# Kernel optimization log

Hardware: AMD Instinct MI355X
Metric: run time of the kernel (lower is better)

The kernel has to match this reference:

```python
import jax, jax.numpy as jnp
import numpy as np

HIDDEN = 128
K = 20
T = 20000
N_PTS = 10011


def setup_inputs() -> dict:
    key = jax.random.key(0)
    ks = jax.random.split(key, 20)
    points = jax.random.normal(ks[0], (N_PTS, 3), dtype=jnp.float32)
    triangles = jax.random.randint(ks[1], (T, 3), 0, N_PTS, dtype=jnp.int64)
    init_probs = jax.random.uniform(ks[2], (T,), dtype=jnp.float32)
    s = 0.05
    inp = {"points": points, "triangles": triangles, "init_probs": init_probs}
    for li in range(3):
        inp[f"W1_{li}"] = jax.random.normal(ks[3 + 4 * li], (HIDDEN, HIDDEN + 9), dtype=jnp.float32) * s
        inp[f"b1_{li}"] = jnp.zeros((HIDDEN,), dtype=jnp.float32)
        inp[f"W2_{li}"] = jax.random.normal(ks[4 + 4 * li], (HIDDEN, HIDDEN), dtype=jnp.float32) * s
        inp[f"b2_{li}"] = jnp.zeros((HIDDEN,), dtype=jnp.float32)
    inp["Wf"] = jax.random.normal(ks[15], (1, HIDDEN), dtype=jnp.float32) * s
    inp["bf"] = jnp.zeros((1,), dtype=jnp.float32)
    return inp


def _geometry(points, triangles):
    tp = points[triangles]                      # [T, 3verts, 3xyz]
    e_ij = tp[:, 0] - tp[:, 1]
    e_ik = tp[:, 0] - tp[:, 2]
    e_jk = tp[:, 1] - tp[:, 2]
    ev = jnp.stack([e_ij, e_ik, e_jk], axis=1)  # [T, 3, 3]
    t_max = jnp.max(ev, axis=1)                 # [T, 3]
    t_min = jnp.min(ev, axis=1)                 # [T, 3]
    bary = tp.mean(axis=1)                      # [T, 3]
    return t_min, t_max, bary


def _knn_edges(bary, k):
    # squared distances (monotone in cdist) -> same k smallest neighbors
    sq = jnp.sum(bary * bary, axis=1)
    d2 = sq[:, None] + sq[None, :] - 2.0 * (bary @ bary.T)   # [T, T]
    _, idx = jax.lax.top_k(-d2, k + 1)                       # k+1 smallest
    nbr = idx[:, 1:]                                         # drop self
    t = bary.shape[0]
    src = jnp.repeat(jnp.arange(t, dtype=nbr.dtype), k)      # [T*k]
    tgt = nbr.reshape(-1)                                    # [T*k]
    return src, tgt


def _triconv(x, t_min, t_max, bary, src, tgt, W1, b1, W2, b2):
    r_n_k = jnp.concatenate(
        [t_min[src] - t_min[tgt], t_max[src] - t_max[tgt], bary[src] - bary[tgt]],
        axis=1,
    )                                                        # [E, 9]
    h = jnp.concatenate([r_n_k, x[src] - x[tgt]], axis=1)    # [E, H+9]
    h = jax.nn.relu(h @ W1.T + b1) @ W2.T + b2               # [E, H]
    return jax.ops.segment_sum(h, src, num_segments=x.shape[0])


def reference(points, triangles, init_probs,
              W1_0, b1_0, W2_0, b2_0,
              W1_1, b1_1, W2_1, b2_1,
              W1_2, b1_2, W2_2, b2_2,
              Wf, bf):
    t_min, t_max, bary = _geometry(points, triangles)
    k = min(K, triangles.shape[0] - 1)
    src, tgt = _knn_edges(bary, k)
    feats = jnp.broadcast_to(init_probs[:, None], (init_probs.shape[0], HIDDEN))
    feats = _triconv(feats, t_min, t_max, bary, src, tgt, W1_0, b1_0, W2_0, b2_0)
    feats = _triconv(feats, t_min, t_max, bary, src, tgt, W1_1, b1_1, W2_1, b2_1)
    feats = _triconv(feats, t_min, t_max, bary, src, tgt, W1_2, b1_2, W2_2, b2_2)
    logits = (feats @ Wf.T + bf)[:, 0]
    return jax.nn.sigmoid(logits)
```

## Files before the change

### kernel.cpp

```cpp
#include <hip/hip_runtime.h>
#include <math.h>

#define T_TRI 20000
#define KNN_K 20
#define H     128

#define WS_GEO    0
#define WS_BQ     (1u<<20)
#define WS_NBR    (2u<<20)
#define WS_RS     (4u<<20)
#define WS_MT     ((4u<<20)+4096)
#define WS_WV     ((4u<<20)+4096+(256u<<10))
#define WS_MM     (5u<<20)
#define WS_CSTART ((5u<<20)+64)
#define WS_CPTR   ((5u<<20)+(32u<<10))
#define WS_HIST   ((5u<<20)+(64u<<10))
#define WS_CID    ((5u<<20)+(128u<<10))
#define WS_CSORT  ((5u<<20)+(256u<<10))
#define WS_OID    ((5u<<20)+(384u<<10))
#define WS_BQS    ((5u<<20)+(512u<<10))
#define WS_WA     ((5u<<20)+(840u<<10))
#define WS_PS     (6u<<20)
#define WS_GEOS   (7u<<20)
#define WS_ZB     (9u<<20)
#define WS_ZA     (20u<<20)

__device__ __forceinline__ float readlane_f(float v, int l) {
    return __uint_as_float(__builtin_amdgcn_readlane(__float_as_uint(v), l));
}
__device__ __forceinline__ unsigned encf(float f) {
    unsigned u = __float_as_uint(f);
    return (u & 0x80000000u) ? ~u : (u | 0x80000000u);
}
__device__ __forceinline__ float decf(unsigned e) {
    unsigned u = (e & 0x80000000u) ? (e & 0x7FFFFFFFu) : ~e;
    return __uint_as_float(u);
}
__device__ __forceinline__ int xcd_swz(int bid, int nwg) {
    int q = nwg >> 3, rm = nwg & 7;
    int x = bid & 7, idx = bid >> 3;
    return (x < rm) ? x*(q+1) + idx : rm*(q+1) + (x-rm)*q + idx;
}

__global__ void grid_init_kernel(unsigned* __restrict__ hist, unsigned* __restrict__ mm) {
    int i = blockIdx.x * 256 + threadIdx.x;
    if (i < 4096) hist[i] = 0u;
    if (i < 3) mm[i] = 0xFFFFFFFFu;
    if (i >= 3 && i < 6) mm[i] = 0u;
}

__global__ void geom_kernel(const float* __restrict__ pts, const int* __restrict__ tris,
                            float* __restrict__ geo, float4* __restrict__ bq,
                            unsigned* __restrict__ mm) {
    int t = blockIdx.x * blockDim.x + threadIdx.x;
    int lane = threadIdx.x & 63;
    bool act = (t < T_TRI);
    int tt = act ? t : 0;
    int i0 = tris[3*tt], i1 = tris[3*tt+1], i2 = tris[3*tt+2];
    float ax = pts[3*i0], ay = pts[3*i0+1], az = pts[3*i0+2];
    float bx = pts[3*i1], by = pts[3*i1+1], bz = pts[3*i1+2];
    float cx = pts[3*i2], cy = pts[3*i2+1], cz = pts[3*i2+2];
    float e0x = ax-bx, e0y = ay-by, e0z = az-bz;
    float e1x = ax-cx, e1y = ay-cy, e1z = az-cz;
    float e2x = bx-cx, e2y = by-cy, e2z = bz-cz;
    float mnx = fminf(fminf(e0x,e1x),e2x), mny = fminf(fminf(e0y,e1y),e2y), mnz = fminf(fminf(e0z,e1z),e2z);
    float mxx = fmaxf(fmaxf(e0x,e1x),e2x), mxy = fmaxf(fmaxf(e0y,e1y),e2y), mxz = fmaxf(fmaxf(e0z,e1z),e2z);
    float gx = (ax+bx+cx)*(1.0f/3.0f), gy = (ay+by+cy)*(1.0f/3.0f), gz = (az+bz+cz)*(1.0f/3.0f);
    float sq = (gx*gx + gy*gy) + gz*gz;
    if (act) {
        float* g = geo + (size_t)t*12;
        g[0]=mnx; g[1]=mny; g[2]=mnz; g[3]=mxx; g[4]=mxy; g[5]=mxz;
        g[6]=gx;  g[7]=gy;  g[8]=gz;  g[9]=0.f; g[10]=0.f; g[11]=0.f;
        bq[t] = make_float4(gx, gy, gz, sq);
    }
    unsigned n0 = act ? encf(gx) : 0xFFFFFFFFu;
    unsigned n1 = act ? encf(gy) : 0xFFFFFFFFu;
    unsigned n2 = act ? encf(gz) : 0xFFFFFFFFu;
    unsigned x0 = act ? encf(gx) : 0u;
    unsigned x1 = act ? encf(gy) : 0u;
    unsigned x2 = act ? encf(gz) : 0u;
#pragma unroll
    for (int off = 32; off >= 1; off >>= 1) {
        n0 = min(n0, (unsigned)__shfl_xor((int)n0, off));
        n1 = min(n1, (unsigned)__shfl_xor((int)n1, off));
        n2 = min(n2, (unsigned)__shfl_xor((int)n2, off));
        x0 = max(x0, (unsigned)__shfl_xor((int)x0, off));
        x1 = max(x1, (unsigned)__shfl_xor((int)x1, off));
        x2 = max(x2, (unsigned)__shfl_xor((int)x2, off));
    }
    if (lane == 0) {
        atomicMin(&mm[0], n0); atomicMin(&mm[1], n1); atomicMin(&mm[2], n2);
        atomicMax(&mm[3], x0); atomicMax(&mm[4], x1); atomicMax(&mm[5], x2);
    }
}

__global__ void cellhist_kernel(const float4* __restrict__ bq, const unsigned* __restrict__ mm,
                                int* __restrict__ cellid, unsigned* __restrict__ hist) {
    int t = blockIdx.x * 256 + threadIdx.x;
    if (t >= T_TRI) return;
    float mnx = decf(mm[0]), mny = decf(mm[1]), mnz = decf(mm[2]);
    float mxx = decf(mm[3]), mxy = decf(mm[4]), mxz = decf(mm[5]);
    float ihx = 16.f / fmaxf(mxx-mnx, 1e-30f);
    float ihy = 16.f / fmaxf(mxy-mny, 1e-30f);
    float ihz = 16.f / fmaxf(mxz-mnz, 1e-30f);
    float4 b = bq[t];
    int ix = min(15, max(0, (int)((b.x-mnx)*ihx)));
    int iy = min(15, max(0, (int)((b.y-mny)*ihy)));
    int iz = min(15, max(0, (int)((b.z-mnz)*ihz)));
    int c = (ix<<8) | (iy<<4) | iz;
    cellid[t] = c;
    atomicAdd(&hist[c], 1u);
}

__global__ __launch_bounds__(1024) void prefix_kernel(const unsigned* __restrict__ hist,
                                                      unsigned* __restrict__ cellstart,
                                                      unsigned* __restrict__ cellptr) {
    __shared__ unsigned sbuf[1024];
    int tid = threadIdx.x;
    uint4 v = ((const uint4*)hist)[tid];
    unsigned mysum = v.x + v.y + v.z + v.w;
    sbuf[tid] = mysum;
    __syncthreads();
    for (int off = 1; off < 1024; off <<= 1) {
        unsigned add = (tid >= off) ? sbuf[tid - off] : 0u;
        __syncthreads();
        sbuf[tid] += add;
        __syncthreads();
    }
    unsigned excl = sbuf[tid] - mysum;
    unsigned p0 = excl, p1 = p0 + v.x, p2 = p1 + v.y, p3 = p2 + v.z;
    cellstart[4*tid+0] = p0; cellstart[4*tid+1] = p1;
    cellstart[4*tid+2] = p2; cellstart[4*tid+3] = p3;
    cellptr[4*tid+0] = p0; cellptr[4*tid+1] = p1;
    cellptr[4*tid+2] = p2; cellptr[4*tid+3] = p3;
    if (tid == 1023) cellstart[4096] = p3 + v.w;
}

__global__ void scatter_kernel(const float4* __restrict__ bq, const int* __restrict__ cellid,
                               const float* __restrict__ geo, const float* __restrict__ probs,
                               unsigned* __restrict__ cellptr, float4* __restrict__ bqs,
                               int* __restrict__ oid, int* __restrict__ csort,
                               float* __restrict__ geo_s, float* __restrict__ probs_s) {
    int t = blockIdx.x * 256 + threadIdx.x;
    if (t >= T_TRI) return;
    int c = cellid[t];
    unsigned p = atomicAdd(&cellptr[c], 1u);
    bqs[p] = bq[t];
    oid[p]  = t;
    csort[p] = c;
    const float4* g4 = (const float4*)geo;
    float4* g4s = (float4*)geo_s;
    g4s[(size_t)p*3+0] = g4[(size_t)t*3+0];
    g4s[(size_t)p*3+1] = g4[(size_t)t*3+1];
    g4s[(size_t)p*3+2] = g4[(size_t)t*3+2];
    probs_s[p] = probs[t];
}

__global__ __launch_bounds__(256) void knn_grid_kernel(const float4* __restrict__ bqs,
        const int* __restrict__ oid, const int* __restrict__ csort,
        const unsigned* __restrict__ cellstart, const unsigned* __restrict__ mm,
        int* __restrict__ nbr) {
    int wave = threadIdx.x >> 6, lane = threadIdx.x & 63;
    int r = blockIdx.x * 4 + wave;
    float4 q = bqs[r];
    int myc = csort[r];
    int cx = (myc>>8)&15, cy = (myc>>4)&15, cz = myc&15;
    float mnx = decf(mm[0]), mny = decf(mm[1]), mnz = decf(mm[2]);
    float hx = (decf(mm[3]) - mnx) * (1.f/16.f);
    float hy = (decf(mm[4]) - mny) * (1.f/16.f);
    float hz = (decf(mm[5]) - mnz) * (1.f/16.f);
    float hmin = fminf(hx, fminf(hy, hz));

    float rd = INFINITY;
    int   ri = 0x7FF00000 | lane;
    int   rk = lane;
    float th = INFINITY;
    int   mi = 0x7FFFFFFF;

#define SCAN_RANGE(RS, RE)                                                          \
    for (unsigned base = (RS); base < (RE); base += 64u) {                          \
        unsigned k = base + (unsigned)lane;                                         \
        bool kv = (k < (RE));                                                       \
        float4 c4 = kv ? bqs[k] : make_float4(INFINITY,INFINITY,INFINITY,INFINITY); \
        int ov = kv ? oid[k] : 0x7FFFFFFF;                                          \
        float dot = fmaf(q.z, c4.z, fmaf(q.y, c4.y, q.x*c4.x));                     \
        float d = (q.w + c4.w) - 2.0f*dot;                                          \
        unsigned long long bal = __ballot(kv && (d <= th));                         \
        while (bal) {                                                               \
            int src = __ffsll(bal) - 1; bal &= bal - 1;                             \
            float dc = readlane_f(d, src);                                          \
            int   jc = __builtin_amdgcn_readlane(ov, src);                          \
            int   kc = (int)base + src;                                             \
            if ((dc < th) || (dc == th && jc < mi)) {                               \
                bool less = (rd < dc) || (rd == dc && ri < jc);                     \
                int pos = __popcll(__ballot(less) & 0x1FFFFFull);                   \
                float sd = __shfl_up(rd, 1);                                        \
                int   si = __shfl_up(ri, 1);                                        \
                int   sk = __shfl_up(rk, 1);                                        \
                if (lane < 21) {                                                    \
                    if (lane == pos)      { rd = dc; ri = jc; rk = kc; }            \
                    else if (lane > pos)  { rd = sd; ri = si; rk = sk; }            \
                }                                                                   \
                th = readlane_f(rd, 20);                                            \
                mi = __builtin_amdgcn_readlane(ri, 20);                             \
            }                                                                       \
        }                                                                           \
    }

#define CELL_BOUND_OK(EX, EY, EZ)                                                   \
    ({  float cl0 = fmaf((float)(EX), hx, mnx);                                     \
        float cm0 = fmaf((float)(EY), hy, mny);                                     \
        float cn0 = fmaf((float)(EZ), hz, mnz);                                     \
        float ddx = fmaxf(fmaxf(cl0 - q.x, q.x - (cl0 + hx)), 0.f);                 \
        float ddy = fmaxf(fmaxf(cm0 - q.y, q.y - (cm0 + hy)), 0.f);                 \
        float ddz = fmaxf(fmaxf(cn0 - q.z, q.z - (cn0 + hz)), 0.f);                 \
        float bnd = fmaf(ddx, ddx, fmaf(ddy, ddy, ddz*ddz));                        \
        (bnd <= th + 1e-3f); })

    {
        unsigned hs = cellstart[myc], he = cellstart[myc + 1];
        unsigned k64 = hs + (unsigned)lane;
        bool kv = (k64 < he);
        float4 c4 = kv ? bqs[k64] : make_float4(INFINITY,INFINITY,INFINITY,INFINITY);
        float dot = fmaf(q.z, c4.z, fmaf(q.y, c4.y, q.x*c4.x));
        float d = (q.w + c4.w) - 2.0f*dot;
        int   jx = kv ? oid[k64] : (0x7FF00000 | lane);
        int   kc = kv ? (int)k64 : 0;
        if (!kv) d = INFINITY;
#pragma unroll
        for (int kk = 2; kk <= 64; kk <<= 1) {
#pragma unroll
            for (int jj = kk >> 1; jj >= 1; jj >>= 1) {
                float od = __shfl_xor(d, jj);
                int   oj = __shfl_xor(jx, jj);
                int   ok = __shfl_xor(kc, jj);
                bool up    = ((lane & kk) == 0);
                bool lower = ((lane & jj) == 0);
                bool less  = (d < od) || (d == od && jx < oj);
                bool keep  = ((lower == up) ? less : !less);
                d = keep ? d : od; jx = keep ? jx : oj; kc = keep ? kc : ok;
            }
        }
        rd = d; ri = jx; rk = kc;
        th = readlane_f(rd, 20);
        mi = __builtin_amdgcn_readlane(ri, 20);
        if (hs + 64u < he) { SCAN_RANGE(hs + 64u, he) }
    }

    for (int w = 1; w <= 15; ++w) {
        if (w == 1) {
            int i = lane;
            bool val = (i < 27) && (i != 13);
            int ii = (i < 27) ? i : 0;
            int dz = ii % 3 - 1, dy = (ii / 3) % 3 - 1, dx = ii / 9 - 1;
            int ex = cx + dx, ey = cy + dy, ez = cz + dz;
            val = val && ex >= 0 && ex < 16 && ey >= 0 && ey < 16 && ez >= 0 && ez < 16;
            int cell = (ex<<8) | (ey<<4) | ez;
            unsigned cs = 0u, ce = 0u;
            if (val) { cs = cellstart[cell]; ce = cellstart[cell+1]; }
            val = val && (cs < ce);
            if (val) val = CELL_BOUND_OK(ex, ey, ez);
            unsigned long long cm = __ballot(val);
            while (cm) {
                int cl = __ffsll(cm) - 1; cm &= cm - 1;
                unsigned s0 = (unsigned)__builtin_amdgcn_readlane((int)cs, cl);
                unsigned e0 = (unsigned)__builtin_amdgcn_readlane((int)ce, cl);
                SCAN_RANGE(s0, e0)
            }
        } else {
            int W = 2*w + 1, W2 = W*W, tot = W*W2;
            for (int b0 = 0; b0 < tot; b0 += 64) {
                int i = b0 + lane;
                bool val = (i < tot);
                int ii = val ? i : 0;
                int dz = ii % W - w, dy = (ii / W) % W - w, dx = ii / W2 - w;
                int cheb = max(abs(dx), max(abs(dy), abs(dz)));
                val = val && (cheb == w);
                int ex = cx + dx, ey = cy + dy, ez = cz + dz;
                val = val && ex >= 0 && ex < 16 && ey >= 0 && ey < 16 && ez >= 0 && ez < 16;
                int cell = (ex<<8) | (ey<<4) | ez;
                unsigned cs = 0u, ce = 0u;
                if (val) { cs = cellstart[cell]; ce = cellstart[cell+1]; }
                val = val && (cs < ce);
                if (val) val = CELL_BOUND_OK(ex, ey, ez);
                unsigned long long cm = __ballot(val);
                while (cm) {
                    int cl = __ffsll(cm) - 1; cm &= cm - 1;
                    unsigned s0 = (unsigned)__builtin_amdgcn_readlane((int)cs, cl);
                    unsigned e0 = (unsigned)__builtin_amdgcn_readlane((int)ce, cl);
                    SCAN_RANGE(s0, e0)
                }
            }
        }
        bool covered = (cx-w <= 0) && (cx+w >= 15) && (cy-w <= 0) && (cy+w >= 15)
                    && (cz-w <= 0) && (cz+w >= 15);
        if (covered) break;
        float bd = (float)w * hmin - 1e-3f;
        if (bd > 0.f && th < bd*bd) break;
    }
#undef CELL_BOUND_OK
#undef SCAN_RANGE
    if (lane >= 1 && lane < 21) nbr[r*KNN_K + lane - 1] = rk;
}

__global__ void prep_kernel(const float* __restrict__ W10, const float* __restrict__ W11,
                            const float* __restrict__ W12,
                            const float* __restrict__ b20, const float* __restrict__ b21,
                            const float* __restrict__ b22, const float* __restrict__ W22,
                            const float* __restrict__ Wf, const float* __restrict__ bf,
                            float* __restrict__ rs, float* __restrict__ WA,
                            float* __restrict__ WV) {
    int f = threadIdx.x;
    float s = 0.f;
    for (int c = 0; c < H; ++c) s += W10[f*137 + 9 + c];
    rs[f] = s;
#pragma unroll
    for (int c = 0; c < 9; ++c) {
        WA[0*1152 + c*128 + f] = W10[f*137 + c];
        WA[1*1152 + c*128 + f] = W11[f*137 + c];
        WA[2*1152 + c*128 + f] = W12[f*137 + c];
    }
    float v0 = 0.f, v1 = 0.f, w2 = 0.f;
    for (int k = 0; k < 128; ++k) {
        v0 = fmaf(W11[f*137 + 9 + k], b20[k], v0);
        v1 = fmaf(W12[f*137 + 9 + k], b21[k], v1);
        w2 = fmaf(Wf[k], W22[k*128 + f], w2);
    }
    WV[f]       = (float)KNN_K * v0;
    WV[128 + f] = (float)KNN_K * v1;
    WV[256 + f] = w2;
    if (f == 0) {
        float cacc = 0.f;
        for (int k = 0; k < 128; ++k) cacc = fmaf(Wf[k], b22[k], cacc);
        WV[384] = (float)KNN_K * cacc + bf[0];
    }
}

__global__ void mfold_kernel(const float* __restrict__ W11, const float* __restrict__ W12,
                             const float* __restrict__ W20, const float* __restrict__ W21,
                             float* __restrict__ MTg) {
    int c = threadIdx.x, f = blockIdx.x, m = blockIdx.y;
    const float* W1 = m ? W12 : W11;
    const float* W2 = m ? W21 : W20;
    float acc = 0.f;
    for (int k = 0; k < 128; ++k)
        acc = fmaf(W1[f*137 + 9 + k], W2[k*128 + c], acc);
    MTg[m*16384 + (c>>2)*512 + f*4 + (c&3)] = acc;
}

__global__ void y0_kernel(const float* __restrict__ ps, const float* __restrict__ rs,
                          const float* __restrict__ WA0, const float* __restrict__ geo_s,
                          float* __restrict__ Z) {
    int bid = xcd_swz(blockIdx.x, gridDim.x);
    int tid = bid * 256 + threadIdx.x;
    int t = tid >> 7, f = tid & 127;
    float acc = ps[t] * rs[f];
#pragma unroll
    for (int c = 0; c < 9; ++c)
        acc = fmaf(WA0[c*128 + f], geo_s[(size_t)t*12 + c], acc);
    Z[tid] = acc;
}

__global__ __launch_bounds__(512) void ef_mid_kernel(const float* __restrict__ Z,
                            const int* __restrict__ nbr, const float* __restrict__ b1,
                            const float* __restrict__ MTg, const float* __restrict__ v,
                            const float* __restrict__ WAn, const float* __restrict__ geo_s,
                            float* __restrict__ Znext) {
    __shared__ float Srow[8][128];
    int wave = threadIdx.x >> 6, lane = threadIdx.x & 63;
    int t0b = xcd_swz(blockIdx.x, gridDim.x) * 8;
    {
        int t = t0b + wave;
        float zsLo = Z[(size_t)t*H + lane]      + b1[lane];
        float zsHi = Z[(size_t)t*H + 64 + lane] + b1[64 + lane];
        float accLo = 0.f, accHi = 0.f;
#pragma unroll
        for (int e = 0; e < KNN_K; ++e) {
            int tg = nbr[t*KNN_K + e];
            accLo += fmaxf(zsLo - Z[(size_t)tg*H + lane],      0.f);
            accHi += fmaxf(zsHi - Z[(size_t)tg*H + 64 + lane], 0.f);
        }
        Srow[wave][lane]    = accLo;
        Srow[wave][64+lane] = accHi;
    }
    __syncthreads();
    int f = threadIdx.x & 127, grp = threadIdx.x >> 7;
    float a0 = v[f], a1 = v[f];
    const int r0_ = grp * 2;
#pragma unroll
    for (int c4 = 0; c4 < 32; ++c4) {
        float4 w = *(const float4*)&MTg[c4*512 + f*4];
        float4 v0 = ((const float4*)Srow[r0_+0])[c4];
        float4 v1 = ((const float4*)Srow[r0_+1])[c4];
        a0 = fmaf(w.x, v0.x, a0); a0 = fmaf(w.y, v0.y, a0);
        a0 = fmaf(w.z, v0.z, a0); a0 = fmaf(w.w, v0.w, a0);
        a1 = fmaf(w.x, v1.x, a1); a1 = fmaf(w.y, v1.y, a1);
        a1 = fmaf(w.z, v1.z, a1); a1 = fmaf(w.w, v1.w, a1);
    }
#pragma unroll
    for (int c = 0; c < 9; ++c) {
        float w = WAn[c*128 + f];
        a0 = fmaf(w, geo_s[(size_t)(t0b + r0_ + 0)*12 + c], a0);
        a1 = fmaf(w, geo_s[(size_t)(t0b + r0_ + 1)*12 + c], a1);
    }
    Znext[(size_t)(t0b+r0_+0)*H + f] = a0;
    Znext[(size_t)(t0b+r0_+1)*H + f] = a1;
}

__global__ __launch_bounds__(256) void ef_head_kernel(const float* __restrict__ Z,
                            const int* __restrict__ nbr, const float* __restrict__ b1,
                            const float* __restrict__ WV, float* __restrict__ out,
                            const int* __restrict__ oid) {
    int wave = threadIdx.x >> 6, lane = threadIdx.x & 63;
    int t = xcd_swz(blockIdx.x, gridDim.x) * 4 + wave;
    float zsLo = Z[(size_t)t*H + lane]      + b1[lane];
    float zsHi = Z[(size_t)t*H + 64 + lane] + b1[64 + lane];
    float accLo = 0.f, accHi = 0.f;
#pragma unroll
    for (int e = 0; e < KNN_K; ++e) {
        int tg = nbr[t*KNN_K + e];
        accLo += fmaxf(zsLo - Z[(size_t)tg*H + lane],      0.f);
        accHi += fmaxf(zsHi - Z[(size_t)tg*H + 64 + lane], 0.f);
    }
    float p = fmaf(accLo, WV[256 + lane], accHi * WV[256 + 64 + lane]);
#pragma unroll
    for (int off = 32; off >= 1; off >>= 1) p += __shfl_xor(p, off);
    if (lane == 0) {
        float z = p + WV[384];
        out[oid[t]] = 1.0f / (1.0f + expf(-z));
    }
}

extern "C" void kernel_launch(void* const* d_in, const int* in_sizes, int n_in,
                              void* d_out, int out_size, void* d_ws, size_t ws_size,
                              hipStream_t stream) {
    (void)in_sizes; (void)n_in; (void)out_size; (void)ws_size;
    const float* pts   = (const float*)d_in[0];
    const int*   tris  = (const int*)d_in[1];
    const float* probs = (const float*)d_in[2];
    const float* W1[3] = {(const float*)d_in[3],  (const float*)d_in[7],  (const float*)d_in[11]};
    const float* b1[3] = {(const float*)d_in[4],  (const float*)d_in[8],  (const float*)d_in[12]};
    const float* W2[3] = {(const float*)d_in[5],  (const float*)d_in[9],  (const float*)d_in[13]};
    const float* b2[3] = {(const float*)d_in[6],  (const float*)d_in[10], (const float*)d_in[14]};
    const float* Wf = (const float*)d_in[15];
    const float* bf = (const float*)d_in[16];
    float* out = (float*)d_out;

    char* ws = (char*)d_ws;
    float*    geo  = (float*)(ws + WS_GEO);
    float4*   bq   = (float4*)(ws + WS_BQ);
    int*      nbr  = (int*)(ws + WS_NBR);
    float*    rs   = (float*)(ws + WS_RS);
    float*    MTg  = (float*)(ws + WS_MT);
    float*    WV   = (float*)(ws + WS_WV);
    unsigned* mm   = (unsigned*)(ws + WS_MM);
    unsigned* cst  = (unsigned*)(ws + WS_CSTART);
    unsigned* cptr = (unsigned*)(ws + WS_CPTR);
    unsigned* hist = (unsigned*)(ws + WS_HIST);
    int*      cid  = (int*)(ws + WS_CID);
    int*      cso  = (int*)(ws + WS_CSORT);
    int*      oid  = (int*)(ws + WS_OID);
    float4*   bqs  = (float4*)(ws + WS_BQS);
    float*    WA   = (float*)(ws + WS_WA);
    float*    ps   = (float*)(ws + WS_PS);
    float*    geos = (float*)(ws + WS_GEOS);
    float*    Za   = (float*)(ws + WS_ZA);
    float*    Zb   = (float*)(ws + WS_ZB);

    grid_init_kernel<<<16, 256, 0, stream>>>(hist, mm);
    geom_kernel<<<(T_TRI+255)/256, 256, 0, stream>>>(pts, tris, geo, bq, mm);
    cellhist_kernel<<<(T_TRI+255)/256, 256, 0, stream>>>(bq, mm, cid, hist);
    prefix_kernel<<<1, 1024, 0, stream>>>(hist, cst, cptr);
    scatter_kernel<<<(T_TRI+255)/256, 256, 0, stream>>>(bq, cid, geo, probs, cptr, bqs, oid, cso, geos, ps);
    knn_grid_kernel<<<T_TRI/4, 256, 0, stream>>>(bqs, oid, cso, cst, mm, nbr);
    prep_kernel<<<1, 128, 0, stream>>>(W1[0], W1[1], W1[2], b2[0], b2[1], b2[2], W2[2], Wf, bf, rs, WA, WV);
    mfold_kernel<<<dim3(128,2), 128, 0, stream>>>(W1[1], W1[2], W2[0], W2[1], MTg);
    y0_kernel<<<(T_TRI*H)/256, 256, 0, stream>>>(ps, rs, WA, geos, Za);
    ef_mid_kernel<<<T_TRI/8, 512, 0, stream>>>(Za, nbr, b1[0], MTg,         WV,       WA + 1*1152, geos, Zb);
    ef_mid_kernel<<<T_TRI/8, 512, 0, stream>>>(Zb, nbr, b1[1], MTg + 16384, WV + 128, WA + 2*1152, geos, Za);
    ef_head_kernel<<<T_TRI/4, 256, 0, stream>>>(Za, nbr, b1[2], WV, out, oid);
}
```

Baseline: 251.6 us.

## Seed KNN from full 3x3x3 neighborhood and merge weight-prep kernels into setup

The KNN kernel now gathers all candidates from the 3x3x3 cell block around the query, using per-column prefix sums across lanes. It sorts the first 64 of them with a bitonic network and inserts the rest through a ballot-filtered insertion. Previously it sorted only the home cell and visited neighbor cells one by one, each with its own bound check. Shells of radius 2 and up are scanned only when the 1-shell bound does not already cover the current threshold. Separately, grid_init, prep and mfold are fused into one setup kernel, removing two launches. The risk is redundant distance work on cells the old bound check would have skipped, plus a per-lane loop over up to 9 columns to find each candidate's source index.

```diff
diff --git a/kernel.cpp b/kernel.cpp
--- a/kernel.cpp
+++ b/kernel.cpp
@@ -42,11 +42,56 @@
     return (x < rm) ? x*(q+1) + idx : rm*(q+1) + (x-rm)*q + idx;
 }
 
-__global__ void grid_init_kernel(unsigned* __restrict__ hist, unsigned* __restrict__ mm) {
-    int i = blockIdx.x * 256 + threadIdx.x;
-    if (i < 4096) hist[i] = 0u;
-    if (i < 3) mm[i] = 0xFFFFFFFFu;
-    if (i >= 3 && i < 6) mm[i] = 0u;
+__global__ void setup_kernel(const float* __restrict__ W10, const float* __restrict__ W11,
+                             const float* __restrict__ W12,
+                             const float* __restrict__ W20, const float* __restrict__ W21,
+                             const float* __restrict__ b20, const float* __restrict__ b21,
+                             const float* __restrict__ b22, const float* __restrict__ W22,
+                             const float* __restrict__ Wf, const float* __restrict__ bf,
+                             unsigned* __restrict__ hist, unsigned* __restrict__ mm,
+                             float* __restrict__ rs, float* __restrict__ WA,
+                             float* __restrict__ WV, float* __restrict__ MTg) {
+    int bx = blockIdx.x, by = blockIdx.y, tid = threadIdx.x;
+    if (bx < 128) {
+        int f = bx, c = tid, m = by;
+        const float* W1 = m ? W12 : W11;
+        const float* W2 = m ? W21 : W20;
+        float acc = 0.f;
+        for (int k = 0; k < 128; ++k)
+            acc = fmaf(W1[f*137 + 9 + k], W2[k*128 + c], acc);
+        MTg[m*16384 + (c>>2)*512 + f*4 + (c&3)] = acc;
+    } else if (bx == 128) {
+        if (by != 0) return;
+        int f = tid;
+        float s = 0.f;
+        for (int c = 0; c < H; ++c) s += W10[f*137 + 9 + c];
+        rs[f] = s;
+#pragma unroll
+        for (int c = 0; c < 9; ++c) {
+            WA[0*1152 + c*128 + f] = W10[f*137 + c];
+            WA[1*1152 + c*128 + f] = W11[f*137 + c];
+            WA[2*1152 + c*128 + f] = W12[f*137 + c];
+        }
+        float v0 = 0.f, v1 = 0.f, w2 = 0.f;
+        for (int k = 0; k < 128; ++k) {
+            v0 = fmaf(W11[f*137 + 9 + k], b20[k], v0);
+            v1 = fmaf(W12[f*137 + 9 + k], b21[k], v1);
+            w2 = fmaf(Wf[k], W22[k*128 + f], w2);
+        }
+        WV[f]       = (float)KNN_K * v0;
+        WV[128 + f] = (float)KNN_K * v1;
+        WV[256 + f] = w2;
+        if (f == 0) {
+            float cacc = 0.f;
+            for (int k = 0; k < 128; ++k) cacc = fmaf(Wf[k], b22[k], cacc);
+            WV[384] = (float)KNN_K * cacc + bf[0];
+        }
+    } else {
+#pragma unroll
+        for (int i = 0; i < 16; ++i) hist[by*2048 + tid*16 + i] = 0u;
+        if (by == 0 && tid < 3) mm[tid] = 0xFFFFFFFFu;
+        if (by == 0 && tid >= 3 && tid < 6) mm[tid] = 0u;
+    }
 }
 
 __global__ void geom_kernel(const float* __restrict__ pts, const int* __restrict__ tris,
@@ -218,56 +263,90 @@
         (bnd <= th + 1e-3f); })
 
     {
-        unsigned hs = cellstart[myc], he = cellstart[myc + 1];
-        unsigned k64 = hs + (unsigned)lane;
-        bool kv = (k64 < he);
-        float4 c4 = kv ? bqs[k64] : make_float4(INFINITY,INFINITY,INFINITY,INFINITY);
-        float dot = fmaf(q.z, c4.z, fmaf(q.y, c4.y, q.x*c4.x));
-        float d = (q.w + c4.w) - 2.0f*dot;
-        int   jx = kv ? oid[k64] : (0x7FF00000 | lane);
-        int   kc = kv ? (int)k64 : 0;
-        if (!kv) d = INFINITY;
-#pragma unroll
-        for (int kk = 2; kk <= 64; kk <<= 1) {
-#pragma unroll
-            for (int jj = kk >> 1; jj >= 1; jj >>= 1) {
-                float od = __shfl_xor(d, jj);
-                int   oj = __shfl_xor(jx, jj);
-                int   ok = __shfl_xor(kc, jj);
-                bool up    = ((lane & kk) == 0);
-                bool lower = ((lane & jj) == 0);
-                bool less  = (d < od) || (d == od && jx < oj);
-                bool keep  = ((lower == up) ? less : !less);
-                d = keep ? d : od; jx = keep ? jx : oj; kc = keep ? kc : ok;
+        int X0 = max(cx-1, 0), X1 = min(cx+1, 15);
+        int Y0 = max(cy-1, 0), Y1 = min(cy+1, 15);
+        int Z0 = max(cz-1, 0), Z1 = min(cz+1, 15);
+        int Wy = Y1 - Y0 + 1;
+        int ncol = (X1 - X0 + 1) * Wy;
+        unsigned ccs = 0u, clen = 0u;
+        if (lane < ncol) {
+            int ex = X0 + lane / Wy, ey = Y0 + lane % Wy;
+            int colb = (ex<<8) | (ey<<4);
+            ccs  = cellstart[colb + Z0];
+            clen = cellstart[colb + Z1 + 1] - ccs;
+        }
+        unsigned inc = clen;
+#pragma unroll
+        for (int off = 1; off < 16; off <<= 1) {
+            unsigned v = (unsigned)__shfl_up((int)inc, off);
+            if (lane >= off) inc += v;
+        }
+        unsigned exc = inc - clen;
+        unsigned L = (unsigned)__builtin_amdgcn_readlane((int)inc, ncol - 1);
+
+        for (unsigned p0 = 0; p0 < L; p0 += 64u) {
+            unsigned p = p0 + (unsigned)lane;
+            bool kv = (p < L);
+            unsigned srcidx = 0u;
+            for (int j = 0; j < ncol; ++j) {
+                unsigned ej = (unsigned)__builtin_amdgcn_readlane((int)exc, j);
+                unsigned lj = (unsigned)__builtin_amdgcn_readlane((int)clen, j);
+                unsigned sj = (unsigned)__builtin_amdgcn_readlane((int)ccs, j);
+                if (p >= ej && p < ej + lj) srcidx = sj + (p - ej);
             }
-        }
-        rd = d; ri = jx; rk = kc;
-        th = readlane_f(rd, 20);
-        mi = __builtin_amdgcn_readlane(ri, 20);
-        if (hs + 64u < he) { SCAN_RANGE(hs + 64u, he) }
-    }
-
-    for (int w = 1; w <= 15; ++w) {
-        if (w == 1) {
-            int i = lane;
-            bool val = (i < 27) && (i != 13);
-            int ii = (i < 27) ? i : 0;
-            int dz = ii % 3 - 1, dy = (ii / 3) % 3 - 1, dx = ii / 9 - 1;
-            int ex = cx + dx, ey = cy + dy, ez = cz + dz;
-            val = val && ex >= 0 && ex < 16 && ey >= 0 && ey < 16 && ez >= 0 && ez < 16;
-            int cell = (ex<<8) | (ey<<4) | ez;
-            unsigned cs = 0u, ce = 0u;
-            if (val) { cs = cellstart[cell]; ce = cellstart[cell+1]; }
-            val = val && (cs < ce);
-            if (val) val = CELL_BOUND_OK(ex, ey, ez);
-            unsigned long long cm = __ballot(val);
-            while (cm) {
-                int cl = __ffsll(cm) - 1; cm &= cm - 1;
-                unsigned s0 = (unsigned)__builtin_amdgcn_readlane((int)cs, cl);
-                unsigned e0 = (unsigned)__builtin_amdgcn_readlane((int)ce, cl);
-                SCAN_RANGE(s0, e0)
+            float4 c4 = kv ? bqs[srcidx] : make_float4(INFINITY,INFINITY,INFINITY,INFINITY);
+            int ov = kv ? oid[srcidx] : (0x7FF00000 | lane);
+            float dot = fmaf(q.z, c4.z, fmaf(q.y, c4.y, q.x*c4.x));
+            float d = (q.w + c4.w) - 2.0f*dot;
+            int kc = kv ? (int)srcidx : lane;
+            if (p0 == 0u) {
+                if (!kv) d = INFINITY;
+#pragma unroll
+                for (int kk = 2; kk <= 64; kk <<= 1) {
+#pragma unroll
+                    for (int jj = kk >> 1; jj >= 1; jj >>= 1) {
+                        float od = __shfl_xor(d, jj);
+                        int   oj = __shfl_xor(ov, jj);
+                        int   ok = __shfl_xor(kc, jj);
+                        bool up    = ((lane & kk) == 0);
+                        bool lower = ((lane & jj) == 0);
+                        bool less  = (d < od) || (d == od && ov < oj);
+                        bool keep  = ((lower == up) ? less : !less);
+                        d = keep ? d : od; ov = keep ? ov : oj; kc = keep ? kc : ok;
+                    }
+                }
+                rd = d; ri = ov; rk = kc;
+                th = readlane_f(rd, 20);
+                mi = __builtin_amdgcn_readlane(ri, 20);
+            } else {
+                unsigned long long bal = __ballot(kv && (d <= th));
+                while (bal) {
+                    int sl = __ffsll(bal) - 1; bal &= bal - 1;
+                    float dc = readlane_f(d, sl);
+                    int   jc = __builtin_amdgcn_readlane(ov, sl);
+                    int   kcc = __builtin_amdgcn_readlane(kc, sl);
+                    if ((dc < th) || (dc == th && jc < mi)) {
+                        bool less = (rd < dc) || (rd == dc && ri < jc);
+                        int pos = __popcll(__ballot(less) & 0x1FFFFFull);
+                        float sd = __shfl_up(rd, 1);
+                        int   si = __shfl_up(ri, 1);
+                        int   sk = __shfl_up(rk, 1);
+                        if (lane < 21) {
+                            if (lane == pos)      { rd = dc; ri = jc; rk = kcc; }
+                            else if (lane > pos)  { rd = sd; ri = si; rk = sk; }
+                        }
+                        th = readlane_f(rd, 20);
+                        mi = __builtin_amdgcn_readlane(ri, 20);
+                    }
+                }
             }
-        } else {
+        }
+    }
+    bool covered1 = (cx-1 <= 0) && (cx+1 >= 15) && (cy-1 <= 0) && (cy+1 >= 15)
+                 && (cz-1 <= 0) && (cz+1 >= 15);
+    float bd1 = hmin - 1e-3f;
+    if (!covered1 && !(bd1 > 0.f && th < bd1*bd1)) {
+        for (int w = 2; w <= 15; ++w) {
             int W = 2*w + 1, W2 = W*W, tot = W*W2;
             for (int b0 = 0; b0 < tot; b0 += 64) {
                 int i = b0 + lane;
@@ -291,61 +370,16 @@
                     SCAN_RANGE(s0, e0)
                 }
             }
-        }
-        bool covered = (cx-w <= 0) && (cx+w >= 15) && (cy-w <= 0) && (cy+w >= 15)
-                    && (cz-w <= 0) && (cz+w >= 15);
-        if (covered) break;
-        float bd = (float)w * hmin - 1e-3f;
-        if (bd > 0.f && th < bd*bd) break;
+            bool covered = (cx-w <= 0) && (cx+w >= 15) && (cy-w <= 0) && (cy+w >= 15)
+                        && (cz-w <= 0) && (cz+w >= 15);
+            if (covered) break;
+            float bd = (float)w * hmin - 1e-3f;
+            if (bd > 0.f && th < bd*bd) break;
+        }
     }
 #undef CELL_BOUND_OK
 #undef SCAN_RANGE
     if (lane >= 1 && lane < 21) nbr[r*KNN_K + lane - 1] = rk;
-}
-
-__global__ void prep_kernel(const float* __restrict__ W10, const float* __restrict__ W11,
-                            const float* __restrict__ W12,
-                            const float* __restrict__ b20, const float* __restrict__ b21,
-                            const float* __restrict__ b22, const float* __restrict__ W22,
-                            const float* __restrict__ Wf, const float* __restrict__ bf,
-                            float* __restrict__ rs, float* __restrict__ WA,
-                            float* __restrict__ WV) {
-    int f = threadIdx.x;
-    float s = 0.f;
-    for (int c = 0; c < H; ++c) s += W10[f*137 + 9 + c];
-    rs[f] = s;
-#pragma unroll
-    for (int c = 0; c < 9; ++c) {
-        WA[0*1152 + c*128 + f] = W10[f*137 + c];
-        WA[1*1152 + c*128 + f] = W11[f*137 + c];
-        WA[2*1152 + c*128 + f] = W12[f*137 + c];
-    }
-    float v0 = 0.f, v1 = 0.f, w2 = 0.f;
-    for (int k = 0; k < 128; ++k) {
-        v0 = fmaf(W11[f*137 + 9 + k], b20[k], v0);
-        v1 = fmaf(W12[f*137 + 9 + k], b21[k], v1);
-        w2 = fmaf(Wf[k], W22[k*128 + f], w2);
-    }
-    WV[f]       = (float)KNN_K * v0;
-    WV[128 + f] = (float)KNN_K * v1;
-    WV[256 + f] = w2;
-    if (f == 0) {
-        float cacc = 0.f;
-        for (int k = 0; k < 128; ++k) cacc = fmaf(Wf[k], b22[k], cacc);
-        WV[384] = (float)KNN_K * cacc + bf[0];
-    }
-}
-
-__global__ void mfold_kernel(const float* __restrict__ W11, const float* __restrict__ W12,
-                             const float* __restrict__ W20, const float* __restrict__ W21,
-                             float* __restrict__ MTg) {
-    int c = threadIdx.x, f = blockIdx.x, m = blockIdx.y;
-    const float* W1 = m ? W12 : W11;
-    const float* W2 = m ? W21 : W20;
-    float acc = 0.f;
-    for (int k = 0; k < 128; ++k)
-        acc = fmaf(W1[f*137 + 9 + k], W2[k*128 + c], acc);
-    MTg[m*16384 + (c>>2)*512 + f*4 + (c&3)] = acc;
 }
 
 __global__ void y0_kernel(const float* __restrict__ ps, const float* __restrict__ rs,
@@ -467,14 +501,14 @@
     float*    Za   = (float*)(ws + WS_ZA);
     float*    Zb   = (float*)(ws + WS_ZB);
 
-    grid_init_kernel<<<16, 256, 0, stream>>>(hist, mm);
+    setup_kernel<<<dim3(130,2), 128, 0, stream>>>(W1[0], W1[1], W1[2], W2[0], W2[1],
+                                                  b2[0], b2[1], b2[2], W2[2], Wf, bf,
+                                                  hist, mm, rs, WA, WV, MTg);
     geom_kernel<<<(T_TRI+255)/256, 256, 0, stream>>>(pts, tris, geo, bq, mm);
     cellhist_kernel<<<(T_TRI+255)/256, 256, 0, stream>>>(bq, mm, cid, hist);
     prefix_kernel<<<1, 1024, 0, stream>>>(hist, cst, cptr);
     scatter_kernel<<<(T_TRI+255)/256, 256, 0, stream>>>(bq, cid, geo, probs, cptr, bqs, oid, cso, geos, ps);
     knn_grid_kernel<<<T_TRI/4, 256, 0, stream>>>(bqs, oid, cso, cst, mm, nbr);
-    prep_kernel<<<1, 128, 0, stream>>>(W1[0], W1[1], W1[2], b2[0], b2[1], b2[2], W2[2], Wf, bf, rs, WA, WV);
-    mfold_kernel<<<dim3(128,2), 128, 0, stream>>>(W1[1], W1[2], W2[0], W2[1], MTg);
     y0_kernel<<<(T_TRI*H)/256, 256, 0, stream>>>(ps, rs, WA, geos, Za);
     ef_mid_kernel<<<T_TRI/8, 512, 0, stream>>>(Za, nbr, b1[0], MTg,         WV,       WA + 1*1152, geos, Zb);
     ef_mid_kernel<<<T_TRI/8, 512, 0, stream>>>(Zb, nbr, b1[1], MTg + 16384, WV + 128, WA + 2*1152, geos, Za);
```

Result: slower. 392.1 us (+55.8%).
